# Performance work log

Measured on AMD Instinct MI355X. Metric: run time of the kernel, lower is better.

The kernel has to match this reference:

```python
import jax, jax.numpy as jnp
import numpy as np

V, D, H, E, C, K = 16000, 1024, 1024, 8, 16, 2  # vocab, embed, expert hidden, n_experts, classes, top_k
B, S = 64, 512
GATE_H = 256


def setup_inputs() -> dict:
    key = jax.random.key(0)
    ks = jax.random.split(key, 11)
    s = lambda i, shape: jax.random.normal(ks[i], shape, jnp.float32) * 0.02
    return dict(
        x=jax.random.randint(ks[0], (B, S), 0, V),
        emb=s(1, (V, D)),                      # shared gating embedding
        gate_w1=s(2, (D, GATE_H)), gate_b1=jnp.zeros((GATE_H,), jnp.float32),
        gate_w2=s(3, (GATE_H, E)), gate_b2=jnp.zeros((E,), jnp.float32),
        exp_emb=s(4, (E, V, D)),               # per-expert embedding tables
        exp_w1=s(5, (E, D, H)), exp_b1=jnp.zeros((E, H), jnp.float32),
        exp_w2=s(6, (E, H, C)), exp_b2=jnp.zeros((E, C), jnp.float32),
    )


def reference(x, emb, gate_w1, gate_b1, gate_w2, gate_b2,
              exp_emb, exp_w1, exp_b1, exp_w2, exp_b2):
    # --- gating: embed, mean-pool over seq, 2-layer MLP, softmax, top-k ---
    pooled = emb[x].mean(axis=1)                                   # [B,D]
    logits = jax.nn.relu(pooled @ gate_w1 + gate_b1) @ gate_w2 + gate_b2  # [B,E]
    probs = jax.nn.softmax(logits, axis=-1)
    rw, idx = jax.lax.top_k(probs, K)                              # [B,K]
    rw = rw / rw.sum(axis=-1, keepdims=True)                       # renormalize

    # --- dispatch: gather each sample's assigned expert params (no per-sample loop) ---
    out = jnp.zeros((x.shape[0], C), jnp.float32)
    for k in range(K):  # tiny fixed loop over top_k
        e = idx[:, k]                                              # [B]
        tok = exp_emb[e[:, None], x]                               # [B,S,D]
        h = jax.nn.relu(jnp.einsum('bsd,bdh->bsh', tok, exp_w1[e]) + exp_b1[e][:, None, :])  # [B,S,H]
        p = h.mean(axis=1)                                         # [B,H]
        eo = jnp.einsum('bh,bhc->bc', p, exp_w2[e]) + exp_b2[e]    # [B,C]
        out = out + rw[:, k:k + 1] * eo
    return out
```

## Files before the change

### kernel.cpp

```cpp
#include <hip/hip_runtime.h>
#include <hip/hip_bf16.h>

#define V_   16000
#define D_   1024
#define H_   1024
#define E_   8
#define C_   16
#define B_   64
#define S_   512
#define GH_  256
#define NPAIR 128

typedef short  bf16x8 __attribute__((ext_vector_type(8)));
typedef ushort u16x8  __attribute__((ext_vector_type(8)));
typedef float  f32x4  __attribute__((ext_vector_type(4)));

static __device__ __forceinline__ ushort f2bf(float f) {
  union { float f; unsigned u; } un; un.f = f;
  unsigned u = un.u;
  return (ushort)((u + 0x7FFFu + ((u >> 16) & 1u)) >> 16);
}

static __device__ __forceinline__ unsigned pk2(float lo, float hi) {
  __hip_bfloat162 h = __float22bfloat162_rn(make_float2(lo, hi));
  unsigned r; __builtin_memcpy(&r, &h, sizeof(r)); return r;
}

static __device__ __forceinline__ void bar_lgkm() {
  asm volatile("s_waitcnt lgkmcnt(0)" ::: "memory");
  __builtin_amdgcn_s_barrier();
}

__global__ void prep_kernel(const float* __restrict__ w1, ushort* __restrict__ w1t,
                            const int* __restrict__ x, const float* __restrict__ emb,
                            float* __restrict__ partial) {
  __shared__ float tile[64][65];
  const int id = blockIdx.x;
  if (id < 2048) {
    const int e = id >> 8, rem = id & 255;
    const int dtile = rem & 15, htile = rem >> 4;
    const int d0 = dtile * 64, h0 = htile * 64;
    const float* src = w1 + (size_t)e * D_ * H_;
    for (int i = threadIdx.x; i < 64 * 64; i += 256) {
      int r = i >> 6, c = i & 63;
      tile[r][c] = src[(size_t)(d0 + r) * H_ + h0 + c];
    }
    __syncthreads();
    for (int i = threadIdx.x; i < 512; i += 256) {
      int chunk = i >> 6, lane = i & 63;
      int kkl = chunk >> 2, htl = chunk & 3;
      int l15 = lane & 15, l16 = lane >> 4;
      u16x8 v;
      #pragma unroll
      for (int j = 0; j < 8; ++j)
        v[j] = f2bf(tile[kkl * 32 + l16 * 8 + j][htl * 16 + l15]);
      size_t off = ((size_t)((e * 32 + dtile * 2 + kkl) * 64 + htile * 4 + htl)) * 512 + lane * 8;
      *reinterpret_cast<u16x8*>(w1t + off) = v;
    }
  } else {
    const int pid = id - 2048;
    const int b = pid >> 3, sb = pid & 7, t = threadIdx.x;
    const int* xr = x + b * S_ + sb * 64;
    float4 acc = make_float4(0.f, 0.f, 0.f, 0.f);
    #pragma unroll 4
    for (int s = 0; s < 64; ++s) {
      const float4* row = reinterpret_cast<const float4*>(emb + (size_t)xr[s] * D_);
      float4 v = row[t];
      acc.x += v.x; acc.y += v.y; acc.z += v.z; acc.w += v.w;
    }
    reinterpret_cast<float4*>(partial + ((size_t)b * 8 + sb) * D_)[t] = acc;
  }
}

__global__ void gate_kernel(const float* __restrict__ partial,
                            const float* __restrict__ gw1, const float* __restrict__ gb1,
                            const float* __restrict__ gw2, const float* __restrict__ gb2,
                            int* __restrict__ ridx, float* __restrict__ rwgt) {
  const int b = blockIdx.x, j = threadIdx.x;
  __shared__ float pl[D_];
  __shared__ float hid[GH_];
  __shared__ float logits[E_];
  for (int d = j; d < D_; d += 256) {
    float s = 0.f;
    #pragma unroll
    for (int sb = 0; sb < 8; ++sb) s += partial[((size_t)b * 8 + sb) * D_ + d];
    pl[d] = s * (1.f / (float)S_);
  }
  __syncthreads();
  float acc = gb1[j];
  for (int d = 0; d < D_; ++d) acc += pl[d] * gw1[d * GH_ + j];
  hid[j] = fmaxf(acc, 0.f);
  __syncthreads();
  if (j < E_) {
    float l = gb2[j];
    for (int i = 0; i < GH_; ++i) l += hid[i] * gw2[i * E_ + j];
    logits[j] = l;
  }
  __syncthreads();
  if (j == 0) {
    int i0 = 0; float v0 = logits[0];
    for (int i = 1; i < E_; ++i) if (logits[i] > v0) { v0 = logits[i]; i0 = i; }
    int i1 = -1; float v1 = -3.0e38f;
    for (int i = 0; i < E_; ++i) {
      if (i == i0) continue;
      if (logits[i] > v1) { v1 = logits[i]; i1 = i; }
    }
    float r1 = expf(v1 - v0);
    float norm = 1.f + r1;
    ridx[b * 2 + 0] = i0;         ridx[b * 2 + 1] = i1;
    rwgt[b * 2 + 0] = 1.f / norm; rwgt[b * 2 + 1] = r1 / norm;
  }
}

__global__ void sort_pairs_kernel(const int* __restrict__ ridx, int* __restrict__ order) {
  __shared__ int se[NPAIR];
  const int t = threadIdx.x;
  se[t] = ridx[t];
  __syncthreads();
  const int e = se[t];
  int rank = 0;
  for (int j = 0; j < NPAIR; ++j) {
    const int ej = se[j];
    rank += (ej < e || (ej == e && j < t)) ? 1 : 0;
  }
  order[rank] = t;
}

__global__ __launch_bounds__(512, 2) void expert_kernel(
    const int* __restrict__ x, const float* __restrict__ exp_emb,
    const ushort* __restrict__ w1t, const float* __restrict__ exp_b1,
    const int* __restrict__ ridx, const int* __restrict__ order,
    float* __restrict__ p_part) {
  const int id     = blockIdx.x;
  const int xcd    = id & 7;
  const int within = id >> 3;
  const int slot   = xcd * 128 + within;
  const int pr     = order[slot >> 3];
  const int sblk   = slot & 7;
  const int b      = pr >> 1;
  const int tid    = threadIdx.x;

  __shared__ __align__(16) ushort lB[64 * 1024];

  const int e = ridx[pr];

  const int grow = tid >> 3, gkq = (tid & 7) * 8;
  const int tok  = x[b * S_ + sblk * 64 + grow];
  const float* gptr = exp_emb + ((size_t)e * V_ + tok) * D_ + gkq;
  const int gdst = grow * 1024 + (gkq ^ ((grow & 7) << 3));

  const int wid = tid >> 6, lane = tid & 63;
  const int l15 = lane & 15, l16 = lane >> 4;
  const int sw  = (l15 & 7) << 3;

  const ushort* aW = w1t + (size_t)e * (32 * 64 * 512) + ((size_t)wid * 4) * 512 + (size_t)lane * 8;
  #define LOADA(kk_, hh_, i_) \
    (*reinterpret_cast<const bf16x8*>(aW + ((size_t)((kk_) * 64 + (hh_) * 32 + (i_))) * 512))

  f32x4 acc[2][4][4];
  #pragma unroll
  for (int hh = 0; hh < 2; ++hh)
    #pragma unroll
    for (int i = 0; i < 4; ++i)
      #pragma unroll
      for (int j = 0; j < 4; ++j) acc[hh][i][j] = (f32x4){0.f, 0.f, 0.f, 0.f};

  f32x4 st[3][2];
  #pragma unroll
  for (int p = 0; p < 3; ++p) {
    st[p][0] = __builtin_nontemporal_load(reinterpret_cast<const f32x4*>(gptr + p * 64));
    st[p][1] = __builtin_nontemporal_load(reinterpret_cast<const f32x4*>(gptr + p * 64 + 4));
  }
  {
    uint4 w;
    w.x = pk2(st[0][0][0], st[0][0][1]); w.y = pk2(st[0][0][2], st[0][0][3]);
    w.z = pk2(st[0][1][0], st[0][1][1]); w.w = pk2(st[0][1][2], st[0][1][3]);
    *reinterpret_cast<uint4*>(&lB[gdst]) = w;
  }
  bar_lgkm();

  #pragma unroll
  for (int s = 0; s < 16; ++s) {
    if (s + 3 < 16) {
      st[s % 3][0] = __builtin_nontemporal_load(reinterpret_cast<const f32x4*>(gptr + (s + 3) * 64));
      st[s % 3][1] = __builtin_nontemporal_load(reinterpret_cast<const f32x4*>(gptr + (s + 3) * 64 + 4));
    }
    #pragma unroll
    for (int ks = 0; ks < 2; ++ks) {
      const int kk = s * 2 + ks;
      const int colk = s * 64 + (((ks << 5) | (l16 << 3)) ^ sw);
      bf16x8 bfr[4];
      #pragma unroll
      for (int j = 0; j < 4; ++j)
        bfr[j] = *reinterpret_cast<const bf16x8*>(&lB[(j * 16 + l15) * 1024 + colk]);
      bf16x8 af0[4], af1[4];
      #pragma unroll
      for (int i = 0; i < 4; ++i) { af0[i] = LOADA(kk, 0, i); af1[i] = LOADA(kk, 1, i); }
      #pragma unroll
      for (int i = 0; i < 4; ++i)
        #pragma unroll
        for (int j = 0; j < 4; ++j)
          acc[0][i][j] = __builtin_amdgcn_mfma_f32_16x16x32_bf16(af0[i], bfr[j], acc[0][i][j], 0, 0, 0);
      #pragma unroll
      for (int i = 0; i < 4; ++i)
        #pragma unroll
        for (int j = 0; j < 4; ++j)
          acc[1][i][j] = __builtin_amdgcn_mfma_f32_16x16x32_bf16(af1[i], bfr[j], acc[1][i][j], 0, 0, 0);
    }
    if (s + 1 < 16) {
      const int p = (s + 1) % 3;
      uint4 w;
      w.x = pk2(st[p][0][0], st[p][0][1]); w.y = pk2(st[p][0][2], st[p][0][3]);
      w.z = pk2(st[p][1][0], st[p][1][1]); w.w = pk2(st[p][1][2], st[p][1][3]);
      *reinterpret_cast<uint4*>(&lB[gdst + (s + 1) * 64]) = w;
    }
    bar_lgkm();
  }

  float* outRow = p_part + (size_t)(sblk * NPAIR + pr) * H_;
  const float* biasE = exp_b1 + e * H_;
  #pragma unroll
  for (int hh = 0; hh < 2; ++hh) {
    #pragma unroll
    for (int i = 0; i < 4; ++i) {
      #pragma unroll
      for (int r = 0; r < 4; ++r) {
        const int h = hh * 512 + wid * 64 + i * 16 + l16 * 4 + r;
        const float bias = biasE[h];
        float v = 0.f;
        #pragma unroll
        for (int j = 0; j < 4; ++j) v += fmaxf(acc[hh][i][j][r] + bias, 0.f);
        #pragma unroll
        for (int m = 1; m < 16; m <<= 1) v += __shfl_xor(v, m);
        if (l15 == 0) outRow[h] = v;
      }
    }
  }
  #undef LOADA
}

__global__ void finalize_kernel(const float* __restrict__ p_part,
                                const int* __restrict__ ridx, const float* __restrict__ rwgt,
                                const float* __restrict__ w2, const float* __restrict__ b2,
                                float* __restrict__ out) {
  const int b = blockIdx.x, t = threadIdx.x;
  const int c = t & 15, g = t >> 4;
  __shared__ float red[16][17];
  float res = 0.f;
  for (int kk = 0; kk < 2; ++kk) {
    const int pr = b * 2 + kk;
    const int e = ridx[pr];
    const float w = rwgt[pr];
    float dot = 0.f;
    for (int h = g; h < H_; h += 16) {
      float pm = 0.f;
      #pragma unroll
      for (int sb = 0; sb < 8; ++sb) pm += p_part[(size_t)(sb * NPAIR + pr) * H_ + h];
      dot += pm * w2[((size_t)e * H_ + h) * C_ + c];
    }
    red[g][c] = dot;
    __syncthreads();
    if (g == 0) {
      float s = 0.f;
      #pragma unroll
      for (int i = 0; i < 16; ++i) s += red[i][c];
      res += w * (s * (1.f / (float)S_) + b2[e * C_ + c]);
    }
    __syncthreads();
  }
  if (g == 0) out[b * C_ + c] = res;
}

extern "C" void kernel_launch(void* const* d_in, const int* in_sizes, int n_in,
                              void* d_out, int out_size, void* d_ws, size_t ws_size,
                              hipStream_t stream) {
  const int*   x    = (const int*)  d_in[0];
  const float* emb  = (const float*)d_in[1];
  const float* gw1  = (const float*)d_in[2];
  const float* gb1  = (const float*)d_in[3];
  const float* gw2  = (const float*)d_in[4];
  const float* gb2  = (const float*)d_in[5];
  const float* eemb = (const float*)d_in[6];
  const float* ew1  = (const float*)d_in[7];
  const float* eb1  = (const float*)d_in[8];
  const float* ew2  = (const float*)d_in[9];
  const float* eb2  = (const float*)d_in[10];
  float* out = (float*)d_out;

  char* ws = (char*)d_ws;
  const size_t OFF_W1T   = 0;
  const size_t OFF_PART  = (size_t)16 << 20;
  const size_t OFF_RIDX  = OFF_PART + ((size_t)2 << 20);
  const size_t OFF_RWGT  = OFF_RIDX + 1024;
  const size_t OFF_ORDER = OFF_RWGT + 1024;
  const size_t OFF_PPART = OFF_ORDER + 1024;

  ushort* w1t    = (ushort*)(ws + OFF_W1T);
  float*  part   = (float*) (ws + OFF_PART);
  int*    ridx   = (int*)   (ws + OFF_RIDX);
  float*  rwgt   = (float*) (ws + OFF_RWGT);
  int*    order  = (int*)   (ws + OFF_ORDER);
  float*  ppart  = (float*) (ws + OFF_PPART);

  prep_kernel<<<dim3(2560), 256, 0, stream>>>(ew1, w1t, x, emb, part);
  gate_kernel<<<dim3(B_), 256, 0, stream>>>(part, gw1, gb1, gw2, gb2, ridx, rwgt);
  sort_pairs_kernel<<<dim3(1), 128, 0, stream>>>(ridx, order);
  expert_kernel<<<dim3(1024), 512, 0, stream>>>(x, eemb, w1t, eb1, ridx, order, ppart);
  finalize_kernel<<<dim3(B_), 256, 0, stream>>>(ppart, ridx, rwgt, ew2, eb2, out);
}
```

Measured before the change: 317.8 us.

## Split expert kernel work across 1024 threads with one H half per wave

The expert kernel moves from 512 threads per block, each wave covering two 512-wide halves of H, to 1024 threads per block, each wave covering a single 64-column slice. Per-thread accumulators are halved, the gather prefetch depth drops from three stages to two, and each thread now stages 4 floats instead of 8. The custom lgkmcnt wait plus barrier is replaced by __syncthreads. This aims to cut register pressure and raise per-block parallelism, at the cost of one 16-wave block per CU (LDS is 128KB per block) and heavier barriers.

```diff
diff --git a/kernel.cpp b/kernel.cpp
--- a/kernel.cpp
+++ b/kernel.cpp
@@ -24,11 +24,6 @@
 static __device__ __forceinline__ unsigned pk2(float lo, float hi) {
   __hip_bfloat162 h = __float22bfloat162_rn(make_float2(lo, hi));
   unsigned r; __builtin_memcpy(&r, &h, sizeof(r)); return r;
-}
-
-static __device__ __forceinline__ void bar_lgkm() {
-  asm volatile("s_waitcnt lgkmcnt(0)" ::: "memory");
-  __builtin_amdgcn_s_barrier();
 }
 
 __global__ void prep_kernel(const float* __restrict__ w1, ushort* __restrict__ w1t,
@@ -126,7 +121,7 @@
   order[rank] = t;
 }
 
-__global__ __launch_bounds__(512, 2) void expert_kernel(
+__global__ __launch_bounds__(1024) void expert_kernel(
     const int* __restrict__ x, const float* __restrict__ exp_emb,
     const ushort* __restrict__ w1t, const float* __restrict__ exp_b1,
     const int* __restrict__ ridx, const int* __restrict__ order,
@@ -144,99 +139,86 @@
 
   const int e = ridx[pr];
 
-  const int grow = tid >> 3, gkq = (tid & 7) * 8;
+  const int grow = tid >> 4, kq4 = (tid & 15) * 4;
   const int tok  = x[b * S_ + sblk * 64 + grow];
-  const float* gptr = exp_emb + ((size_t)e * V_ + tok) * D_ + gkq;
-  const int gdst = grow * 1024 + (gkq ^ ((grow & 7) << 3));
+  const float* gptr = exp_emb + ((size_t)e * V_ + tok) * D_ + kq4;
+  const int swz  = (grow & 7) << 3;
+  const int gdst = grow * 1024 + (((kq4 & ~7) ^ swz) + (kq4 & 7));
 
   const int wid = tid >> 6, lane = tid & 63;
   const int l15 = lane & 15, l16 = lane >> 4;
   const int sw  = (l15 & 7) << 3;
 
-  const ushort* aW = w1t + (size_t)e * (32 * 64 * 512) + ((size_t)wid * 4) * 512 + (size_t)lane * 8;
-  #define LOADA(kk_, hh_, i_) \
-    (*reinterpret_cast<const bf16x8*>(aW + ((size_t)((kk_) * 64 + (hh_) * 32 + (i_))) * 512))
-
-  f32x4 acc[2][4][4];
+  const ushort* aLane = w1t + (size_t)e * (32 * 64 * 512)
+                        + ((size_t)wid * 4) * 512 + (size_t)lane * 8;
+  #define LOADA(kk_, i_) \
+    (*reinterpret_cast<const bf16x8*>(aLane + ((size_t)((kk_) * 64 + (i_))) * 512))
+
+  f32x4 acc[4][4];
   #pragma unroll
-  for (int hh = 0; hh < 2; ++hh)
-    #pragma unroll
-    for (int i = 0; i < 4; ++i)
-      #pragma unroll
-      for (int j = 0; j < 4; ++j) acc[hh][i][j] = (f32x4){0.f, 0.f, 0.f, 0.f};
-
-  f32x4 st[3][2];
-  #pragma unroll
-  for (int p = 0; p < 3; ++p) {
-    st[p][0] = __builtin_nontemporal_load(reinterpret_cast<const f32x4*>(gptr + p * 64));
-    st[p][1] = __builtin_nontemporal_load(reinterpret_cast<const f32x4*>(gptr + p * 64 + 4));
-  }
+  for (int i = 0; i < 4; ++i)
+    #pragma unroll
+    for (int j = 0; j < 4; ++j) acc[i][j] = (f32x4){0.f, 0.f, 0.f, 0.f};
+
+  f32x4 stP[2];
+  stP[0] = __builtin_nontemporal_load(reinterpret_cast<const f32x4*>(gptr));
   {
-    uint4 w;
-    w.x = pk2(st[0][0][0], st[0][0][1]); w.y = pk2(st[0][0][2], st[0][0][3]);
-    w.z = pk2(st[0][1][0], st[0][1][1]); w.w = pk2(st[0][1][2], st[0][1][3]);
-    *reinterpret_cast<uint4*>(&lB[gdst]) = w;
-  }
-  bar_lgkm();
+    uint2 w;
+    w.x = pk2(stP[0][0], stP[0][1]); w.y = pk2(stP[0][2], stP[0][3]);
+    *reinterpret_cast<uint2*>(&lB[gdst]) = w;
+  }
+  stP[1] = __builtin_nontemporal_load(reinterpret_cast<const f32x4*>(gptr + 64));
+  __syncthreads();
 
   #pragma unroll
   for (int s = 0; s < 16; ++s) {
-    if (s + 3 < 16) {
-      st[s % 3][0] = __builtin_nontemporal_load(reinterpret_cast<const f32x4*>(gptr + (s + 3) * 64));
-      st[s % 3][1] = __builtin_nontemporal_load(reinterpret_cast<const f32x4*>(gptr + (s + 3) * 64 + 4));
+    const int cur = s & 1;
+    if (s + 2 < 16) {
+      stP[cur] = __builtin_nontemporal_load(
+          reinterpret_cast<const f32x4*>(gptr + (s + 2) * 64));
     }
     #pragma unroll
     for (int ks = 0; ks < 2; ++ks) {
       const int kk = s * 2 + ks;
       const int colk = s * 64 + (((ks << 5) | (l16 << 3)) ^ sw);
-      bf16x8 bfr[4];
+      bf16x8 bfr[4], af[4];
       #pragma unroll
       for (int j = 0; j < 4; ++j)
         bfr[j] = *reinterpret_cast<const bf16x8*>(&lB[(j * 16 + l15) * 1024 + colk]);
-      bf16x8 af0[4], af1[4];
-      #pragma unroll
-      for (int i = 0; i < 4; ++i) { af0[i] = LOADA(kk, 0, i); af1[i] = LOADA(kk, 1, i); }
+      #pragma unroll
+      for (int i = 0; i < 4; ++i) af[i] = LOADA(kk, i);
       #pragma unroll
       for (int i = 0; i < 4; ++i)
         #pragma unroll
         for (int j = 0; j < 4; ++j)
-          acc[0][i][j] = __builtin_amdgcn_mfma_f32_16x16x32_bf16(af0[i], bfr[j], acc[0][i][j], 0, 0, 0);
-      #pragma unroll
-      for (int i = 0; i < 4; ++i)
-        #pragma unroll
-        for (int j = 0; j < 4; ++j)
-          acc[1][i][j] = __builtin_amdgcn_mfma_f32_16x16x32_bf16(af1[i], bfr[j], acc[1][i][j], 0, 0, 0);
+          acc[i][j] = __builtin_amdgcn_mfma_f32_16x16x32_bf16(af[i], bfr[j], acc[i][j], 0, 0, 0);
     }
     if (s + 1 < 16) {
-      const int p = (s + 1) % 3;
-      uint4 w;
-      w.x = pk2(st[p][0][0], st[p][0][1]); w.y = pk2(st[p][0][2], st[p][0][3]);
-      w.z = pk2(st[p][1][0], st[p][1][1]); w.w = pk2(st[p][1][2], st[p][1][3]);
-      *reinterpret_cast<uint4*>(&lB[gdst + (s + 1) * 64]) = w;
-    }
-    bar_lgkm();
-  }
+      uint2 w;
+      w.x = pk2(stP[cur ^ 1][0], stP[cur ^ 1][1]);
+      w.y = pk2(stP[cur ^ 1][2], stP[cur ^ 1][3]);
+      *reinterpret_cast<uint2*>(&lB[gdst + (s + 1) * 64]) = w;
+    }
+    __syncthreads();
+  }
+  #undef LOADA
 
   float* outRow = p_part + (size_t)(sblk * NPAIR + pr) * H_;
   const float* biasE = exp_b1 + e * H_;
   #pragma unroll
-  for (int hh = 0; hh < 2; ++hh) {
-    #pragma unroll
-    for (int i = 0; i < 4; ++i) {
-      #pragma unroll
-      for (int r = 0; r < 4; ++r) {
-        const int h = hh * 512 + wid * 64 + i * 16 + l16 * 4 + r;
-        const float bias = biasE[h];
-        float v = 0.f;
-        #pragma unroll
-        for (int j = 0; j < 4; ++j) v += fmaxf(acc[hh][i][j][r] + bias, 0.f);
-        #pragma unroll
-        for (int m = 1; m < 16; m <<= 1) v += __shfl_xor(v, m);
-        if (l15 == 0) outRow[h] = v;
-      }
-    }
-  }
-  #undef LOADA
+  for (int i = 0; i < 4; ++i) {
+    #pragma unroll
+    for (int r = 0; r < 4; ++r) {
+      const int h = wid * 64 + i * 16 + l16 * 4 + r;
+      const float bias = biasE[h];
+      float v = 0.f;
+      #pragma unroll
+      for (int j = 0; j < 4; ++j) v += fmaxf(acc[i][j][r] + bias, 0.f);
+      #pragma unroll
+      for (int m = 1; m < 16; m <<= 1) v += __shfl_xor(v, m);
+      if (l15 == 0) outRow[h] = v;
+    }
+  }
 }
 
 __global__ void finalize_kernel(const float* __restrict__ p_part,
@@ -305,6 +287,6 @@
   prep_kernel<<<dim3(2560), 256, 0, stream>>>(ew1, w1t, x, emb, part);
   gate_kernel<<<dim3(B_), 256, 0, stream>>>(part, gw1, gb1, gw2, gb2, ridx, rwgt);
   sort_pairs_kernel<<<dim3(1), 128, 0, stream>>>(ridx, order);
-  expert_kernel<<<dim3(1024), 512, 0, stream>>>(x, eemb, w1t, eb1, ridx, order, ppart);
+  expert_kernel<<<dim3(1024), 1024, 0, stream>>>(x, eemb, w1t, eb1, ridx, order, ppart);
   finalize_kernel<<<dim3(B_), 256, 0, stream>>>(ppart, ridx, rwgt, ew2, eb2, out);
 }
```

New measurement: 256.7 us, median of 3. 19.2% less time.
